# Kernel optimization log

Measured on AMD Instinct MI355X. Metric: run time of the kernel, lower is better.

Reference implementation:

```python
import jax, jax.numpy as jnp
import numpy as np

N, E = 50000, 800000
IN_C, OUT_C, H, EW_DIM = 64, 32, 4, 16
NEG_SLOPE = 0.2


def setup_inputs() -> dict:
    key = jax.random.key(0)
    ks = jax.random.split(key, 10)
    x = jax.random.normal(ks[0], (N, IN_C), dtype=jnp.float32)
    src = jax.random.randint(ks[1], (E,), 0, N)
    dst = jax.random.randint(ks[2], (E,), 0, N)
    edge_index = jnp.stack([src, dst]).astype(jnp.int64)
    edge_weight = jax.random.normal(ks[3], (E, EW_DIM), dtype=jnp.float32)
    # GATConv params: lin weight [IN_C, H*OUT_C], bias [H*OUT_C], att_src/att_dst [H, OUT_C]
    s = 1.0 / np.sqrt(IN_C)
    W = jax.random.uniform(ks[4], (IN_C, H * OUT_C), minval=-s, maxval=s, dtype=jnp.float32)
    b = jnp.zeros((H * OUT_C,), dtype=jnp.float32)
    att_src = jax.random.normal(ks[5], (H, OUT_C), dtype=jnp.float32) * 0.1
    att_dst = jax.random.normal(ks[6], (H, OUT_C), dtype=jnp.float32) * 0.1
    # edge_weight_lin params: [EW_DIM, H], [H]
    se = 1.0 / np.sqrt(EW_DIM)
    Wl = jax.random.uniform(ks[7], (EW_DIM, H), minval=-se, maxval=se, dtype=jnp.float32)
    bl = jax.random.uniform(ks[8], (H,), minval=-se, maxval=se, dtype=jnp.float32)
    return {"x": x, "edge_index": edge_index, "edge_weight": edge_weight,
            "W": W, "b": b, "att_src": att_src, "att_dst": att_dst,
            "Wl": Wl, "bl": bl}


def gate_forward(x, edge_index, edge_weight, W, b, att_src, att_dst, Wl, bl):
    n = x.shape[0]
    h = (x @ W).reshape(n, H, OUT_C)                      # [N,H,C]
    a_src = jnp.einsum('nhc,hc->nh', h, att_src)          # [N,H]
    a_dst = jnp.einsum('nhc,hc->nh', h, att_dst)          # [N,H]
    # per-edge attention logits from edge weights (softmax over heads)
    edge_alpha = jax.nn.softmax(edge_weight @ Wl + bl, axis=1)  # [E,H]
    # add self loops (GATConv default add_self_loops=True, fill_value='mean')
    loop = jnp.arange(n)
    src = jnp.concatenate([edge_index[0], loop])
    dst = jnp.concatenate([edge_index[1], loop])
    loop_alpha = jnp.broadcast_to(edge_alpha.mean(axis=0), (n, H))
    ea = jnp.concatenate([edge_alpha, loop_alpha], axis=0)      # [E+N,H]
    # per-edge logits: gather src/dst contributions + edge term
    alpha = jax.nn.leaky_relu(a_src[src] + a_dst[dst] + ea, NEG_SLOPE)  # [E+N,H]
    # segment softmax grouped by destination node
    amax = jax.ops.segment_max(alpha, dst, num_segments=n)
    ex = jnp.exp(alpha - amax[dst])
    denom = jax.ops.segment_sum(ex, dst, num_segments=n)
    alpha = ex / (denom[dst] + 1e-16)                     # [E+N,H]
    # weighted messages, scatter-add aggregate
    msg = h[src] * alpha[:, :, None]                      # [E+N,H,C]
    out = jax.ops.segment_sum(msg, dst, num_segments=n)   # [N,H,C]
    return out.reshape(n, H * OUT_C) + b


def reference(x, edge_index, edge_weight, W, b, att_src, att_dst, Wl, bl):
    return gate_forward(x, edge_index, edge_weight, W, b, att_src, att_dst, Wl, bl)
```

## Files before the change

kernel.cpp:

```cpp
#include <hip/hip_runtime.h>
#include <math.h>

#define IN_C 64
#define HC 128
#define NHEAD 4
#define EWD 16
#define NEG 0.2f

__device__ __forceinline__ float lrelu(float v) { return v > 0.f ? v : NEG * v; }

__global__ void k_feat(const float* __restrict__ x, const float* __restrict__ W,
                       const float* __restrict__ att_s, const float* __restrict__ att_d,
                       float* __restrict__ h, float* __restrict__ a_src, float* __restrict__ a_dst,
                       int N) {
    __shared__ float Ws[IN_C * HC];
    __shared__ float xs[4][IN_C];
    const int tid = threadIdx.x;
    {
        const float4* W4 = (const float4*)W;
        float4* Ws4 = (float4*)Ws;
#pragma unroll
        for (int i = 0; i < (IN_C * HC / 4) / 128; ++i)
            Ws4[tid + i * 128] = W4[tid + i * 128];
    }
    const float as = att_s[tid];
    const float ad = att_d[tid];
    const int head = tid >> 5;
    for (int base = blockIdx.x * 4; base < N; base += gridDim.x * 4) {
        const int nrows = min(4, N - base);
        __syncthreads();
        if (tid < 64) {
            int r = tid >> 4, q = tid & 15;
            if (r < nrows)
                ((float4*)&xs[r][0])[q] = ((const float4*)(x + (size_t)(base + r) * IN_C))[q];
        }
        __syncthreads();
        for (int r = 0; r < nrows; ++r) {
            float acc = 0.f;
#pragma unroll
            for (int c = 0; c < IN_C; ++c)
                acc = fmaf(xs[r][c], Ws[c * HC + tid], acc);
            const int n = base + r;
            h[(size_t)n * HC + tid] = acc;
            float ps = acc * as, pd = acc * ad;
#pragma unroll
            for (int off = 16; off; off >>= 1) {
                ps += __shfl_xor(ps, off, 32);
                pd += __shfl_xor(pd, off, 32);
            }
            if ((tid & 31) == 0) {
                a_src[n * NHEAD + head] = ps;
                a_dst[n * NHEAD + head] = pd;
            }
        }
    }
}

__global__ void k_count(const int* __restrict__ dst, int* __restrict__ deg, int E) {
    int e = blockIdx.x * 256 + threadIdx.x;
    if (e < E) atomicAdd(&deg[dst[e]], 1);
}

__global__ void k_scan1(const int* __restrict__ deg, int* __restrict__ part, int N) {
    const int b = blockIdx.x, tid = threadIdx.x;
    int base = b * 1024 + tid * 4;
    int s = 0;
#pragma unroll
    for (int k = 0; k < 4; ++k) { int i = base + k; if (i < N) s += deg[i]; }
#pragma unroll
    for (int off = 32; off; off >>= 1) s += __shfl_xor(s, off, 64);
    __shared__ int ls[4];
    if ((tid & 63) == 0) ls[tid >> 6] = s;
    __syncthreads();
    if (tid == 0) part[b] = ls[0] + ls[1] + ls[2] + ls[3];
}

__global__ void k_scan2(int* part, int nb) {
    const int tid = threadIdx.x;
    int orig = (tid < nb) ? part[tid] : 0;
    int v = orig;
#pragma unroll
    for (int off = 1; off < 64; off <<= 1) {
        int t = __shfl_up(v, off, 64);
        if (tid >= off) v += t;
    }
    if (tid < nb) part[tid] = v - orig;
}

__global__ void k_scan3(const int* __restrict__ deg, const int* __restrict__ part,
                        int* __restrict__ rowptr, int* __restrict__ cursor, int N, int E) {
    const int b = blockIdx.x, tid = threadIdx.x;
    int base = b * 1024 + tid * 4;
    int d[4]; int s = 0;
#pragma unroll
    for (int k = 0; k < 4; ++k) { int i = base + k; d[k] = (i < N) ? deg[i] : 0; s += d[k]; }
    int v = s;
#pragma unroll
    for (int off = 1; off < 64; off <<= 1) {
        int t = __shfl_up(v, off, 64);
        if ((tid & 63) >= off) v += t;
    }
    __shared__ int wsum[4];
    if ((tid & 63) == 63) wsum[tid >> 6] = v;
    __syncthreads();
    int waveoff = 0;
    const int w = tid >> 6;
    for (int k = 0; k < w; ++k) waveoff += wsum[k];
    int excl = v - s + waveoff + part[b];
#pragma unroll
    for (int k = 0; k < 4; ++k) {
        int i = base + k;
        if (i < N) { rowptr[i] = excl; cursor[i] = excl; }
        excl += d[k];
    }
    if (b == 0 && tid == 0) rowptr[N] = E;
}

__global__ void k_fill(const int* __restrict__ src, const int* __restrict__ dst,
                       const float* __restrict__ ew, const float* __restrict__ Wl,
                       const float* __restrict__ bl,
                       const float* __restrict__ a_src, const float* __restrict__ a_dst,
                       int* __restrict__ cursor, int2* __restrict__ csr,
                       float4* __restrict__ ex_edge, float* __restrict__ partial, int E) {
    __shared__ float sW[EWD * NHEAD];
    __shared__ float sb[NHEAD];
    __shared__ float sred[4][4];
    const int tid = threadIdx.x;
    if (tid < EWD * NHEAD) sW[tid] = Wl[tid];
    if (tid < NHEAD) sb[tid] = bl[tid];
    __syncthreads();
    float loc[4] = {0.f, 0.f, 0.f, 0.f};
    const int e = blockIdx.x * 256 + tid;
    if (e < E) {
        const float4* w4 = (const float4*)(ew + (size_t)e * EWD);
        float v[4];
#pragma unroll
        for (int hh = 0; hh < 4; ++hh) v[hh] = sb[hh];
#pragma unroll
        for (int q = 0; q < 4; ++q) {
            float4 t = w4[q];
            float tv[4] = {t.x, t.y, t.z, t.w};
#pragma unroll
            for (int k = 0; k < 4; ++k)
#pragma unroll
                for (int hh = 0; hh < 4; ++hh)
                    v[hh] = fmaf(tv[k], sW[(q * 4 + k) * 4 + hh], v[hh]);
        }
        float m = fmaxf(fmaxf(v[0], v[1]), fmaxf(v[2], v[3]));
        float s = 0.f;
#pragma unroll
        for (int hh = 0; hh < 4; ++hh) { v[hh] = __expf(v[hh] - m); s += v[hh]; }
        float inv = 1.f / s;
#pragma unroll
        for (int hh = 0; hh < 4; ++hh) { v[hh] *= inv; loc[hh] += v[hh]; }
        const int sn = src[e], dn = dst[e];
        float4 as = ((const float4*)a_src)[sn];
        float4 ad = ((const float4*)a_dst)[dn];
        float4 ex;
        ex.x = __expf(lrelu(as.x + ad.x + v[0]));
        ex.y = __expf(lrelu(as.y + ad.y + v[1]));
        ex.z = __expf(lrelu(as.z + ad.z + v[2]));
        ex.w = __expf(lrelu(as.w + ad.w + v[3]));
        ex_edge[e] = ex;
        int slot = atomicAdd(&cursor[dn], 1);
        csr[slot] = make_int2(sn, e);
    }
    const int w = tid >> 6;
#pragma unroll
    for (int hh = 0; hh < 4; ++hh) {
        float v = loc[hh];
#pragma unroll
        for (int off = 32; off; off >>= 1) v += __shfl_xor(v, off, 64);
        if ((tid & 63) == 0) sred[w][hh] = v;
    }
    __syncthreads();
    if (tid < 4)
        partial[blockIdx.x * 4 + tid] =
            sred[0][tid] + sred[1][tid] + sred[2][tid] + sred[3][tid];
}

__global__ void k_red(const float* __restrict__ partial, float* __restrict__ asum, int nb) {
    const int tid = threadIdx.x;
    const int w = tid >> 6, lane = tid & 63;
    float s = 0.f;
    for (int b = lane; b < nb; b += 64) s += partial[b * 4 + w];
#pragma unroll
    for (int off = 32; off; off >>= 1) s += __shfl_xor(s, off, 64);
    if (lane == 0) asum[w] = s;
}

__global__ void k_agg(const float* __restrict__ h, const int* __restrict__ rowptr,
                      const int2* __restrict__ csr, const float4* __restrict__ ex_edge,
                      const float* __restrict__ a_src, const float* __restrict__ a_dst,
                      const float* __restrict__ asum, const float* __restrict__ bias,
                      float* __restrict__ out, int N, int E) {
    const int d = blockIdx.x;
    const int tid = threadIdx.x;
    const int head = tid >> 5;
    __shared__ int ssrc[32];
    __shared__ float sex[32][4];
    const int r0 = rowptr[d], r1 = rowptr[d + 1];
    float acc = 0.f, den = 0.f;
    for (int base = r0; base < r1; base += 32) {
        const int cnt = min(32, r1 - base);
        __syncthreads();
        if (tid < cnt) {
            int2 ce = csr[base + tid];
            ssrc[tid] = ce.x;
            float4 e4 = ex_edge[ce.y];
            sex[tid][0] = e4.x; sex[tid][1] = e4.y; sex[tid][2] = e4.z; sex[tid][3] = e4.w;
        }
        __syncthreads();
        int k = 0;
        for (; k + 4 <= cnt; k += 4) {
            const int s0 = ssrc[k], s1 = ssrc[k+1], s2 = ssrc[k+2], s3 = ssrc[k+3];
            const float e0 = sex[k][head], e1 = sex[k+1][head],
                        e2 = sex[k+2][head], e3 = sex[k+3][head];
            const float h0 = h[(size_t)s0 * HC + tid];
            const float h1 = h[(size_t)s1 * HC + tid];
            const float h2 = h[(size_t)s2 * HC + tid];
            const float h3 = h[(size_t)s3 * HC + tid];
            acc = fmaf(h0, e0, acc); den += e0;
            acc = fmaf(h1, e1, acc); den += e1;
            acc = fmaf(h2, e2, acc); den += e2;
            acc = fmaf(h3, e3, acc); den += e3;
        }
        for (; k < cnt; ++k) {
            const int s = ssrc[k];
            const float ex = sex[k][head];
            acc = fmaf(h[(size_t)s * HC + tid], ex, acc);
            den += ex;
        }
    }
    const float mean = asum[head] * (1.0f / (float)E);
    float l = lrelu(a_src[d * NHEAD + head] + a_dst[d * NHEAD + head] + mean);
    const float exl = __expf(l);
    acc = fmaf(h[(size_t)d * HC + tid], exl, acc);
    den += exl;
    out[(size_t)d * HC + tid] = acc / (den + 1e-16f) + bias[tid];
}

extern "C" void kernel_launch(void* const* d_in, const int* in_sizes, int n_in,
                              void* d_out, int out_size, void* d_ws, size_t ws_size,
                              hipStream_t stream) {
    const float* x     = (const float*)d_in[0];
    const int*   ei    = (const int*)d_in[1];
    const float* ew    = (const float*)d_in[2];
    const float* W     = (const float*)d_in[3];
    const float* bias  = (const float*)d_in[4];
    const float* att_s = (const float*)d_in[5];
    const float* att_d = (const float*)d_in[6];
    const float* Wl    = (const float*)d_in[7];
    const float* bl    = (const float*)d_in[8];
    const int N = in_sizes[0] / IN_C;
    const int E = in_sizes[1] / 2;
    const int* src = ei;
    const int* dst = ei + E;
    float* out = (float*)d_out;

    const int FILL_BLOCKS = (E + 255) / 256;

    float* ws = (float*)d_ws;
    size_t off = 0;
    float* h      = ws + off; off += (size_t)N * HC;
    float* a_src  = ws + off; off += (size_t)N * NHEAD;
    float* a_dst  = ws + off; off += (size_t)N * NHEAD;
    int*   deg    = (int*)(ws + off); off += N;
    float* asum   = ws + off; off += 4;
    int*   part   = (int*)(ws + off); off += 64;
    int*   rowptr = (int*)(ws + off); off += (size_t)N + 4;
    int*   cursor = (int*)(ws + off); off += N;
    int2*  csr    = (int2*)(ws + off); off += (size_t)E * 2;
    float4* ex_edge = (float4*)(ws + off); off += (size_t)E * 4;
    float* partial= ws + off; off += (size_t)FILL_BLOCKS * 4;

    hipMemsetAsync(deg, 0, (size_t)N * 4, stream);

    k_feat<<<2048, 128, 0, stream>>>(x, W, att_s, att_d, h, a_src, a_dst, N);
    k_count<<<(E + 255) / 256, 256, 0, stream>>>(dst, deg, E);
    const int nb = (N + 1023) / 1024;
    k_scan1<<<nb, 256, 0, stream>>>(deg, part, N);
    k_scan2<<<1, 64, 0, stream>>>(part, nb);
    k_scan3<<<nb, 256, 0, stream>>>(deg, part, rowptr, cursor, N, E);
    k_fill<<<FILL_BLOCKS, 256, 0, stream>>>(src, dst, ew, Wl, bl, a_src, a_dst,
                                            cursor, csr, ex_edge, partial, E);
    k_red<<<1, 256, 0, stream>>>(partial, asum, FILL_BLOCKS);
    k_agg<<<N, 128, 0, stream>>>(h, rowptr, csr, ex_edge, a_src, a_dst,
                                 asum, bias, out, N, E);
}
```

Measured before the change: 332.6 us.

## Store node features in bf16 and pack edge weights into CSR records

Node features h are now written as bf16 and widened back to float on each gather in the aggregation kernel, which halves the bytes of the dominant random gather. The per-edge exp values are packed as bf16 pairs into a 16-byte CSR record next to the source index, so the aggregation no longer does a second indirect load into a separate ex_edge array. The cost is reduced precision in h and in the attention weights, which may push the output past tolerance.

```diff
diff --git a/kernel.cpp b/kernel.cpp
--- a/kernel.cpp
+++ b/kernel.cpp
@@ -8,11 +8,19 @@
 #define NEG 0.2f
 
 __device__ __forceinline__ float lrelu(float v) { return v > 0.f ? v : NEG * v; }
+__device__ __forceinline__ unsigned short f2b(float f) {
+    unsigned int u = __float_as_uint(f);
+    unsigned int r = ((u >> 16) & 1u) + 0x7fffu;
+    return (unsigned short)((u + r) >> 16);
+}
+__device__ __forceinline__ float b2f(unsigned int lo16) {
+    return __uint_as_float(lo16 << 16);
+}
 
 __global__ void k_feat(const float* __restrict__ x, const float* __restrict__ W,
                        const float* __restrict__ att_s, const float* __restrict__ att_d,
-                       float* __restrict__ h, float* __restrict__ a_src, float* __restrict__ a_dst,
-                       int N) {
+                       unsigned short* __restrict__ h_bf, float* __restrict__ a_src,
+                       float* __restrict__ a_dst, int N) {
     __shared__ float Ws[IN_C * HC];
     __shared__ float xs[4][IN_C];
     const int tid = threadIdx.x;
@@ -41,7 +49,7 @@
             for (int c = 0; c < IN_C; ++c)
                 acc = fmaf(xs[r][c], Ws[c * HC + tid], acc);
             const int n = base + r;
-            h[(size_t)n * HC + tid] = acc;
+            h_bf[(size_t)n * HC + tid] = f2b(acc);
             float ps = acc * as, pd = acc * ad;
 #pragma unroll
             for (int off = 16; off; off >>= 1) {
@@ -120,8 +128,8 @@
                        const float* __restrict__ ew, const float* __restrict__ Wl,
                        const float* __restrict__ bl,
                        const float* __restrict__ a_src, const float* __restrict__ a_dst,
-                       int* __restrict__ cursor, int2* __restrict__ csr,
-                       float4* __restrict__ ex_edge, float* __restrict__ partial, int E) {
+                       int* __restrict__ cursor, uint4* __restrict__ csr,
+                       float* __restrict__ partial, int E) {
     __shared__ float sW[EWD * NHEAD];
     __shared__ float sb[NHEAD];
     __shared__ float sred[4][4];
@@ -156,14 +164,17 @@
         const int sn = src[e], dn = dst[e];
         float4 as = ((const float4*)a_src)[sn];
         float4 ad = ((const float4*)a_dst)[dn];
-        float4 ex;
-        ex.x = __expf(lrelu(as.x + ad.x + v[0]));
-        ex.y = __expf(lrelu(as.y + ad.y + v[1]));
-        ex.z = __expf(lrelu(as.z + ad.z + v[2]));
-        ex.w = __expf(lrelu(as.w + ad.w + v[3]));
-        ex_edge[e] = ex;
+        unsigned int e0 = f2b(__expf(lrelu(as.x + ad.x + v[0])));
+        unsigned int e1 = f2b(__expf(lrelu(as.y + ad.y + v[1])));
+        unsigned int e2 = f2b(__expf(lrelu(as.z + ad.z + v[2])));
+        unsigned int e3 = f2b(__expf(lrelu(as.w + ad.w + v[3])));
+        uint4 rec;
+        rec.x = (unsigned int)sn;
+        rec.y = e0 | (e1 << 16);
+        rec.z = e2 | (e3 << 16);
+        rec.w = 0u;
         int slot = atomicAdd(&cursor[dn], 1);
-        csr[slot] = make_int2(sn, e);
+        csr[slot] = rec;
     }
     const int w = tid >> 6;
 #pragma unroll
@@ -189,8 +200,8 @@
     if (lane == 0) asum[w] = s;
 }
 
-__global__ void k_agg(const float* __restrict__ h, const int* __restrict__ rowptr,
-                      const int2* __restrict__ csr, const float4* __restrict__ ex_edge,
+__global__ void k_agg(const unsigned short* __restrict__ h_bf, const int* __restrict__ rowptr,
+                      const uint4* __restrict__ csr,
                       const float* __restrict__ a_src, const float* __restrict__ a_dst,
                       const float* __restrict__ asum, const float* __restrict__ bias,
                       float* __restrict__ out, int N, int E) {
@@ -205,10 +216,12 @@
         const int cnt = min(32, r1 - base);
         __syncthreads();
         if (tid < cnt) {
-            int2 ce = csr[base + tid];
-            ssrc[tid] = ce.x;
-            float4 e4 = ex_edge[ce.y];
-            sex[tid][0] = e4.x; sex[tid][1] = e4.y; sex[tid][2] = e4.z; sex[tid][3] = e4.w;
+            uint4 rec = csr[base + tid];
+            ssrc[tid] = (int)rec.x;
+            sex[tid][0] = b2f(rec.y & 0xffffu);
+            sex[tid][1] = b2f(rec.y >> 16);
+            sex[tid][2] = b2f(rec.z & 0xffffu);
+            sex[tid][3] = b2f(rec.z >> 16);
         }
         __syncthreads();
         int k = 0;
@@ -216,10 +229,10 @@
             const int s0 = ssrc[k], s1 = ssrc[k+1], s2 = ssrc[k+2], s3 = ssrc[k+3];
             const float e0 = sex[k][head], e1 = sex[k+1][head],
                         e2 = sex[k+2][head], e3 = sex[k+3][head];
-            const float h0 = h[(size_t)s0 * HC + tid];
-            const float h1 = h[(size_t)s1 * HC + tid];
-            const float h2 = h[(size_t)s2 * HC + tid];
-            const float h3 = h[(size_t)s3 * HC + tid];
+            const float h0 = b2f(h_bf[(size_t)s0 * HC + tid]);
+            const float h1 = b2f(h_bf[(size_t)s1 * HC + tid]);
+            const float h2 = b2f(h_bf[(size_t)s2 * HC + tid]);
+            const float h3 = b2f(h_bf[(size_t)s3 * HC + tid]);
             acc = fmaf(h0, e0, acc); den += e0;
             acc = fmaf(h1, e1, acc); den += e1;
             acc = fmaf(h2, e2, acc); den += e2;
@@ -228,14 +241,14 @@
         for (; k < cnt; ++k) {
             const int s = ssrc[k];
             const float ex = sex[k][head];
-            acc = fmaf(h[(size_t)s * HC + tid], ex, acc);
+            acc = fmaf(b2f(h_bf[(size_t)s * HC + tid]), ex, acc);
             den += ex;
         }
     }
     const float mean = asum[head] * (1.0f / (float)E);
     float l = lrelu(a_src[d * NHEAD + head] + a_dst[d * NHEAD + head] + mean);
     const float exl = __expf(l);
-    acc = fmaf(h[(size_t)d * HC + tid], exl, acc);
+    acc = fmaf(b2f(h_bf[(size_t)d * HC + tid]), exl, acc);
     den += exl;
     out[(size_t)d * HC + tid] = acc / (den + 1e-16f) + bias[tid];
 }
@@ -262,7 +275,7 @@
 
     float* ws = (float*)d_ws;
     size_t off = 0;
-    float* h      = ws + off; off += (size_t)N * HC;
+    unsigned short* h_bf = (unsigned short*)(ws + off); off += (size_t)N * HC / 2;
     float* a_src  = ws + off; off += (size_t)N * NHEAD;
     float* a_dst  = ws + off; off += (size_t)N * NHEAD;
     int*   deg    = (int*)(ws + off); off += N;
@@ -270,21 +283,20 @@
     int*   part   = (int*)(ws + off); off += 64;
     int*   rowptr = (int*)(ws + off); off += (size_t)N + 4;
     int*   cursor = (int*)(ws + off); off += N;
-    int2*  csr    = (int2*)(ws + off); off += (size_t)E * 2;
-    float4* ex_edge = (float4*)(ws + off); off += (size_t)E * 4;
+    uint4* csr    = (uint4*)(ws + off); off += (size_t)E * 4;
     float* partial= ws + off; off += (size_t)FILL_BLOCKS * 4;
 
     hipMemsetAsync(deg, 0, (size_t)N * 4, stream);
 
-    k_feat<<<2048, 128, 0, stream>>>(x, W, att_s, att_d, h, a_src, a_dst, N);
+    k_feat<<<2048, 128, 0, stream>>>(x, W, att_s, att_d, h_bf, a_src, a_dst, N);
     k_count<<<(E + 255) / 256, 256, 0, stream>>>(dst, deg, E);
     const int nb = (N + 1023) / 1024;
     k_scan1<<<nb, 256, 0, stream>>>(deg, part, N);
     k_scan2<<<1, 64, 0, stream>>>(part, nb);
     k_scan3<<<nb, 256, 0, stream>>>(deg, part, rowptr, cursor, N, E);
     k_fill<<<FILL_BLOCKS, 256, 0, stream>>>(src, dst, ew, Wl, bl, a_src, a_dst,
-                                            cursor, csr, ex_edge, partial, E);
+                                            cursor, csr, partial, E);
     k_red<<<1, 256, 0, stream>>>(partial, asum, FILL_BLOCKS);
-    k_agg<<<N, 128, 0, stream>>>(h, rowptr, csr, ex_edge, a_src, a_dst,
+    k_agg<<<N, 128, 0, stream>>>(h_bf, rowptr, csr, a_src, a_dst,
                                  asum, bias, out, N, E);
 }
```

After: 300.8 us. 1.11x faster.
